# Performance work log

Measured on AMD Instinct MI355X. Metric: run time of the kernel, lower is better.

Reference implementation:

```python
import jax, jax.numpy as jnp
import numpy as np

HIDDEN = 2048
TOKENS = 16384


def setup_inputs() -> dict:
    key = jax.random.key(0)
    kx, kw, kb, kg, kbe = jax.random.split(key, 5)
    x = jax.random.normal(kx, (TOKENS, HIDDEN), dtype=jnp.float32)
    # LayerNorm affine params
    ln_gamma = jnp.ones((HIDDEN,), dtype=jnp.float32)
    ln_beta = jnp.zeros((HIDDEN,), dtype=jnp.float32)
    # Linear params (PyTorch default init scale ~ U(-1/sqrt(d), 1/sqrt(d)))
    bound = 1.0 / np.sqrt(HIDDEN)
    W = jax.random.uniform(kw, (HIDDEN, HIDDEN), minval=-bound, maxval=bound, dtype=jnp.float32)
    b = jax.random.uniform(kb, (HIDDEN,), minval=-bound, maxval=bound, dtype=jnp.float32)
    return {"x": x, "ln_gamma": ln_gamma, "ln_beta": ln_beta, "W": W, "b": b}


def reference(x, ln_gamma, ln_beta, W, b):
    eps = 1e-5
    mu = jnp.mean(x, axis=-1, keepdims=True)
    var = jnp.mean(jnp.square(x - mu), axis=-1, keepdims=True)
    xn = (x - mu) * jax.lax.rsqrt(var + eps) * ln_gamma + ln_beta
    # Linear: y = xn @ W^T + b (W stored as [out, in] like torch)
    y = jnp.einsum('td,od->to', xn, W) + b
    # torch F.gelu default = exact erf gelu
    return jax.nn.gelu(y, approximate=False)
```

## Files before the change

kernel.cpp:

```cpp
#include <hip/hip_runtime.h>
#include <math.h>

#define TOKENS 16384
#define HIDDEN 2048
#define BM 256
#define BN 256
#define BK 64
#define NT (HIDDEN / BK)

typedef __attribute__((ext_vector_type(4))) float f32x4;
typedef __attribute__((ext_vector_type(8))) short s16x8;

__device__ __forceinline__ unsigned short f2bf(float f) {
  unsigned int u = __float_as_uint(f);
  u += 0x7fffu + ((u >> 16) & 1u);
  return (unsigned short)(u >> 16);
}

__device__ __forceinline__ float fast_gelu(float y) {
  float t = y * fmaf(y * y, 0.044715f, 1.0f);
  float e = __builtin_amdgcn_exp2f(-2.3022082f * t);
  return y * __builtin_amdgcn_rcpf(1.0f + e);
}

__global__ __launch_bounds__(256) void wconv_kernel(const float* __restrict__ W,
                                                    unsigned short* __restrict__ Wb) {
  const int n4 = (HIDDEN * HIDDEN) / 4;
  for (int i = blockIdx.x * 256 + threadIdx.x; i < n4; i += gridDim.x * 256) {
    float4 v = *(const float4*)(W + (size_t)i * 4);
    ushort4 o;
    o.x = f2bf(v.x); o.y = f2bf(v.y); o.z = f2bf(v.z); o.w = f2bf(v.w);
    *(ushort4*)(Wb + (size_t)i * 4) = o;
  }
}

__global__ __launch_bounds__(256) void ln_kernel(const float* __restrict__ x,
                                                 const float* __restrict__ gamma,
                                                 const float* __restrict__ beta,
                                                 unsigned short* __restrict__ xn) {
  const int row = blockIdx.x;
  const int t = threadIdx.x;
  const int wave = t >> 6, lane = t & 63;
  const float* xr = x + (size_t)row * HIDDEN + t * 8;
  float4 v0 = *(const float4*)(xr);
  float4 v1 = *(const float4*)(xr + 4);
  float xv[8] = {v0.x, v0.y, v0.z, v0.w, v1.x, v1.y, v1.z, v1.w};

  float s = 0.f, ss = 0.f;
#pragma unroll
  for (int j = 0; j < 8; ++j) { s += xv[j]; ss = fmaf(xv[j], xv[j], ss); }

#pragma unroll
  for (int off = 32; off > 0; off >>= 1) {
    s += __shfl_xor(s, off, 64);
    ss += __shfl_xor(ss, off, 64);
  }
  __shared__ float rs[4], rss[4];
  if (lane == 0) { rs[wave] = s; rss[wave] = ss; }
  __syncthreads();
  s = rs[0] + rs[1] + rs[2] + rs[3];
  ss = rss[0] + rss[1] + rss[2] + rss[3];

  const float mean = s * (1.0f / HIDDEN);
  const float var = ss * (1.0f / HIDDEN) - mean * mean;
  const float rstd = rsqrtf(var + 1e-5f);

  float4 g0 = *(const float4*)(gamma + t * 8);
  float4 g1 = *(const float4*)(gamma + t * 8 + 4);
  float4 b0 = *(const float4*)(beta + t * 8);
  float4 b1 = *(const float4*)(beta + t * 8 + 4);
  float gv[8] = {g0.x, g0.y, g0.z, g0.w, g1.x, g1.y, g1.z, g1.w};
  float bv[8] = {b0.x, b0.y, b0.z, b0.w, b1.x, b1.y, b1.z, b1.w};

  union { unsigned short h[8]; uint4 q; } pk;
#pragma unroll
  for (int j = 0; j < 8; ++j)
    pk.h[j] = f2bf((xv[j] - mean) * rstd * gv[j] + bv[j]);
  *(uint4*)(xn + (size_t)row * HIDDEN + t * 8) = pk.q;
}


#define GLOAD(gp, lp) __builtin_amdgcn_global_load_lds( \
    (const __attribute__((address_space(1))) unsigned int*)(gp), \
    (__attribute__((address_space(3))) unsigned int*)(lp), 16, 0, 0)

__global__ __launch_bounds__(512, 1) void gemm_kernel(const unsigned short* __restrict__ A,
                                                      const unsigned short* __restrict__ B,
                                                      const float* __restrict__ bias,
                                                      float* __restrict__ out) {
  __shared__ __attribute__((aligned(16))) char lds[131072];

  const int tid = threadIdx.x;
  const int lane = tid & 63;
  const int wave = tid >> 6;
  const int fr = lane & 15, hi = lane >> 4;

  const int wg = blockIdx.x;
  const int swz = (wg & 7) * 64 + (wg >> 3);
  const int tm = swz >> 3, tn = swz & 7;
  const int row0 = tm * BM, col0 = tn * BN;

  const int wmi = wave >> 2;
  const int wni = wave & 3;
  const int hB = wni >> 1, gB = wni & 1;

  const int rho = tid >> 3, sig = tid & 7;
  const int colgrp = ((sig ^ (rho & 7)) << 3);
  const unsigned short* Ap = A + (size_t)(row0 + rho) * HIDDEN + colgrp;
  const unsigned short* Bp = B + (size_t)(col0 + ((rho >> 5) << 6) + (rho & 31)) * HIDDEN + colgrp;
  const int ldsWaveOff = wave << 10;

  const int s0 = ((hi ^ (fr & 7)) << 4);
  const int s1 = (((4 + hi) ^ (fr & 7)) << 4);
  const int aRowB = fr << 7;
  const int bRowB = (((gB << 5) + fr) << 7);

  auto stageA = [&](int tt, int bufd, int qm) {
    const int tc = tt < NT ? tt : NT - 1;
    const unsigned short* g = Ap + (size_t)(qm << 6) * HIDDEN + tc * BK;
    GLOAD(g, lds + ((((bufd << 2) | qm) << 13)) + ldsWaveOff);
    GLOAD(g + (size_t)128 * HIDDEN, lds + ((((bufd << 2) | 2 | qm) << 13)) + ldsWaveOff);
  };
  auto stageB = [&](int tt, int bufd, int qn) {
    const int tc = tt < NT ? tt : NT - 1;
    const unsigned short* g = Bp + (size_t)(qn << 5) * HIDDEN + tc * BK;
    GLOAD(g, lds + 65536 + ((((bufd << 2) | qn) << 13)) + ldsWaveOff);
    GLOAD(g + (size_t)128 * HIDDEN, lds + 65536 + ((((bufd << 2) | 2 | qn) << 13)) + ldsWaveOff);
  };

  f32x4 acc[2][4][4] = {};
  s16x8 a[4][2], b[2][2];

  stageA(0, 0, 0); stageB(0, 0, 1); stageA(0, 0, 1); stageB(0, 0, 0);
  stageA(1, 1, 0); stageB(1, 1, 1);
  asm volatile("s_waitcnt vmcnt(4)" ::: "memory");
  __builtin_amdgcn_s_barrier();

  for (int t = 0; t < NT; ++t) {
    const int buf = t & 1;
    const char* Abase = lds + (((buf << 2) | (wmi << 1)) << 13);
    const char* Bbase = lds + 65536 + (((buf << 2) | (hB << 1)) << 13);

#pragma unroll
    for (int mi = 0; mi < 4; ++mi) {
      a[mi][0] = *(const s16x8*)(Abase + mi * 2048 + aRowB + s0);
      a[mi][1] = *(const s16x8*)(Abase + mi * 2048 + aRowB + s1);
    }
#pragma unroll
    for (int nj = 0; nj < 2; ++nj) {
      b[nj][0] = *(const s16x8*)(Bbase + nj * 2048 + bRowB + s0);
      b[nj][1] = *(const s16x8*)(Bbase + nj * 2048 + bRowB + s1);
    }
    stageA(t + 1, buf ^ 1, 1);
    asm volatile("s_waitcnt lgkmcnt(8)" ::: "memory");
    __builtin_amdgcn_s_barrier();
    asm volatile("s_waitcnt lgkmcnt(0)" ::: "memory");
    __builtin_amdgcn_s_setprio(1);
#pragma unroll
    for (int mi = 0; mi < 4; ++mi)
#pragma unroll
      for (int nj = 0; nj < 2; ++nj)
#pragma unroll
        for (int kk = 0; kk < 2; ++kk)
          acc[0][mi][nj] = __builtin_amdgcn_mfma_f32_16x16x32_bf16(a[mi][kk], b[nj][kk], acc[0][mi][nj], 0, 0, 0);
    __builtin_amdgcn_s_setprio(0);
    __builtin_amdgcn_s_barrier();

#pragma unroll
    for (int nj = 0; nj < 2; ++nj) {
      b[nj][0] = *(const s16x8*)(Bbase + 8192 + nj * 2048 + bRowB + s0);
      b[nj][1] = *(const s16x8*)(Bbase + 8192 + nj * 2048 + bRowB + s1);
    }
    stageB(t + 1, buf ^ 1, 0);
    __builtin_amdgcn_s_barrier();
    asm volatile("s_waitcnt lgkmcnt(0)" ::: "memory");
    __builtin_amdgcn_s_setprio(1);
#pragma unroll
    for (int mi = 0; mi < 4; ++mi)
#pragma unroll
      for (int nj = 0; nj < 2; ++nj)
#pragma unroll
        for (int kk = 0; kk < 2; ++kk)
          acc[0][mi][2 + nj] = __builtin_amdgcn_mfma_f32_16x16x32_bf16(a[mi][kk], b[nj][kk], acc[0][mi][2 + nj], 0, 0, 0);
    __builtin_amdgcn_s_setprio(0);
    __builtin_amdgcn_s_barrier();

#pragma unroll
    for (int mi = 0; mi < 4; ++mi) {
      a[mi][0] = *(const s16x8*)(Abase + 8192 + mi * 2048 + aRowB + s0);
      a[mi][1] = *(const s16x8*)(Abase + 8192 + mi * 2048 + aRowB + s1);
    }
    stageA(t + 2, buf, 0);
    asm volatile("s_waitcnt lgkmcnt(4)" ::: "memory");
    __builtin_amdgcn_s_barrier();
    asm volatile("s_waitcnt lgkmcnt(0)" ::: "memory");
    __builtin_amdgcn_s_setprio(1);
#pragma unroll
    for (int mi = 0; mi < 4; ++mi)
#pragma unroll
      for (int nj = 0; nj < 2; ++nj)
#pragma unroll
        for (int kk = 0; kk < 2; ++kk)
          acc[1][mi][2 + nj] = __builtin_amdgcn_mfma_f32_16x16x32_bf16(a[mi][kk], b[nj][kk], acc[1][mi][2 + nj], 0, 0, 0);
    __builtin_amdgcn_s_setprio(0);
    __builtin_amdgcn_s_barrier();

#pragma unroll
    for (int nj = 0; nj < 2; ++nj) {
      b[nj][0] = *(const s16x8*)(Bbase + nj * 2048 + bRowB + s0);
      b[nj][1] = *(const s16x8*)(Bbase + nj * 2048 + bRowB + s1);
    }
    stageB(t + 2, buf, 1);
    asm volatile("s_waitcnt vmcnt(4)" ::: "memory");
    __builtin_amdgcn_s_barrier();
    asm volatile("s_waitcnt lgkmcnt(0)" ::: "memory");
    __builtin_amdgcn_s_setprio(1);
#pragma unroll
    for (int mi = 0; mi < 4; ++mi)
#pragma unroll
      for (int nj = 0; nj < 2; ++nj)
#pragma unroll
        for (int kk = 0; kk < 2; ++kk)
          acc[1][mi][nj] = __builtin_amdgcn_mfma_f32_16x16x32_bf16(a[mi][kk], b[nj][kk], acc[1][mi][nj], 0, 0, 0);
    __builtin_amdgcn_s_setprio(0);
    __builtin_amdgcn_s_barrier();
  }

  asm volatile("s_waitcnt vmcnt(0)" ::: "memory");

  float bcol[4];
#pragma unroll
  for (int ni = 0; ni < 4; ++ni)
    bcol[ni] = bias[col0 + (wni << 6) + ni * 16 + fr];

#pragma unroll
  for (int qm = 0; qm < 2; ++qm)
#pragma unroll
    for (int mi = 0; mi < 4; ++mi)
#pragma unroll
      for (int ni = 0; ni < 4; ++ni) {
        const int c = col0 + (wni << 6) + ni * 16 + fr;
#pragma unroll
        for (int j = 0; j < 4; ++j) {
          const int r = row0 + wmi * 128 + qm * 64 + mi * 16 + hi * 4 + j;
          float y = acc[qm][mi][ni][j] + bcol[ni];
          out[(size_t)r * HIDDEN + c] = fast_gelu(y);
        }
      }
}

extern "C" void kernel_launch(void* const* d_in, const int* in_sizes, int n_in,
                              void* d_out, int out_size, void* d_ws, size_t ws_size,
                              hipStream_t stream) {
  const float* x     = (const float*)d_in[0];
  const float* gamma = (const float*)d_in[1];
  const float* beta  = (const float*)d_in[2];
  const float* W     = (const float*)d_in[3];
  const float* bias  = (const float*)d_in[4];
  float* out = (float*)d_out;

  unsigned short* xn = (unsigned short*)d_ws;
  unsigned short* wb = (unsigned short*)((char*)d_ws + (size_t)TOKENS * HIDDEN * 2);

  hipLaunchKernelGGL(wconv_kernel, dim3(1024), dim3(256), 0, stream, W, wb);
  hipLaunchKernelGGL(ln_kernel, dim3(TOKENS), dim3(256), 0, stream, x, gamma, beta, xn);
  hipLaunchKernelGGL(gemm_kernel, dim3((TOKENS / BM) * (HIDDEN / BN)), dim3(512), 0, stream,
                     xn, wb, bias, out);
}
```

Measured before the change: 176.2 us.

## Make GEMM workgroups process two row tiles sequentially with continuous pipeline

The GEMM grid is halved so each workgroup computes two output tiles, 8192 rows apart, sharing the same column block. The K-loop runs over both tiles back to back, keeping the LDS prefetch pipeline going across the boundary, and the first tile's epilogue is flushed mid-loop. This targets the tail effect of 512 single-wave workgroups on 256 CUs (exactly two waves) and the per-tile pipeline warmup. The cost is that the first tile's epilogue stores now stall the pipeline mid-loop, and the swizzle mapping changes.

```diff
diff --git a/kernel.cpp b/kernel.cpp
--- a/kernel.cpp
+++ b/kernel.cpp
@@ -7,6 +7,8 @@
 #define BN 256
 #define BK 64
 #define NT (HIDDEN / BK)
+#define NVT (2 * NT)
+#define PASS_ROWS (32 * BM)
 
 typedef __attribute__((ext_vector_type(4))) float f32x4;
 typedef __attribute__((ext_vector_type(8))) short s16x8;
@@ -96,7 +98,7 @@
   const int fr = lane & 15, hi = lane >> 4;
 
   const int wg = blockIdx.x;
-  const int swz = (wg & 7) * 64 + (wg >> 3);
+  const int swz = (wg & 7) * 32 + (wg >> 3);
   const int tm = swz >> 3, tn = swz & 7;
   const int row0 = tm * BM, col0 = tn * BN;
 
@@ -115,28 +117,50 @@
   const int aRowB = fr << 7;
   const int bRowB = (((gB << 5) + fr) << 7);
 
-  auto stageA = [&](int tt, int bufd, int qm) {
-    const int tc = tt < NT ? tt : NT - 1;
-    const unsigned short* g = Ap + (size_t)(qm << 6) * HIDDEN + tc * BK;
+  auto stageA = [&](int vt, int bufd, int qm) {
+    const int vc = vt < NVT ? vt : NVT - 1;
+    const unsigned short* g = Ap + (size_t)(vc >> 5) * ((size_t)PASS_ROWS * HIDDEN)
+                                 + (size_t)(qm << 6) * HIDDEN + (vc & 31) * BK;
     GLOAD(g, lds + ((((bufd << 2) | qm) << 13)) + ldsWaveOff);
     GLOAD(g + (size_t)128 * HIDDEN, lds + ((((bufd << 2) | 2 | qm) << 13)) + ldsWaveOff);
   };
-  auto stageB = [&](int tt, int bufd, int qn) {
-    const int tc = tt < NT ? tt : NT - 1;
-    const unsigned short* g = Bp + (size_t)(qn << 5) * HIDDEN + tc * BK;
+  auto stageB = [&](int vt, int bufd, int qn) {
+    const int vc = vt < NVT ? vt : NVT - 1;
+    const unsigned short* g = Bp + (size_t)(qn << 5) * HIDDEN + (vc & 31) * BK;
     GLOAD(g, lds + 65536 + ((((bufd << 2) | qn) << 13)) + ldsWaveOff);
     GLOAD(g + (size_t)128 * HIDDEN, lds + 65536 + ((((bufd << 2) | 2 | qn) << 13)) + ldsWaveOff);
   };
 
   f32x4 acc[2][4][4] = {};
   s16x8 a[4][2], b[2][2];
+
+  auto flush = [&](int pass) {
+    float bcol[4];
+#pragma unroll
+    for (int ni = 0; ni < 4; ++ni)
+      bcol[ni] = bias[col0 + (wni << 6) + ni * 16 + fr];
+#pragma unroll
+    for (int qm = 0; qm < 2; ++qm)
+#pragma unroll
+      for (int mi = 0; mi < 4; ++mi)
+#pragma unroll
+        for (int ni = 0; ni < 4; ++ni) {
+          const int c = col0 + (wni << 6) + ni * 16 + fr;
+#pragma unroll
+          for (int j = 0; j < 4; ++j) {
+            const int r = row0 + pass * PASS_ROWS + wmi * 128 + qm * 64 + mi * 16 + hi * 4 + j;
+            float y = acc[qm][mi][ni][j] + bcol[ni];
+            out[(size_t)r * HIDDEN + c] = fast_gelu(y);
+          }
+        }
+  };
 
   stageA(0, 0, 0); stageB(0, 0, 1); stageA(0, 0, 1); stageB(0, 0, 0);
   stageA(1, 1, 0); stageB(1, 1, 1);
   asm volatile("s_waitcnt vmcnt(4)" ::: "memory");
   __builtin_amdgcn_s_barrier();
 
-  for (int t = 0; t < NT; ++t) {
+  for (int t = 0; t < NVT; ++t) {
     const int buf = t & 1;
     const char* Abase = lds + (((buf << 2) | (wmi << 1)) << 13);
     const char* Bbase = lds + 65536 + (((buf << 2) | (hB << 1)) << 13);
@@ -224,29 +248,21 @@
           acc[1][mi][nj] = __builtin_amdgcn_mfma_f32_16x16x32_bf16(a[mi][kk], b[nj][kk], acc[1][mi][nj], 0, 0, 0);
     __builtin_amdgcn_s_setprio(0);
     __builtin_amdgcn_s_barrier();
+
+    if (t == NT - 1) {
+      flush(0);
+#pragma unroll
+      for (int qm = 0; qm < 2; ++qm)
+#pragma unroll
+        for (int mi = 0; mi < 4; ++mi)
+#pragma unroll
+          for (int ni = 0; ni < 4; ++ni)
+            acc[qm][mi][ni] = (f32x4){0.f, 0.f, 0.f, 0.f};
+    }
   }
 
   asm volatile("s_waitcnt vmcnt(0)" ::: "memory");
-
-  float bcol[4];
-#pragma unroll
-  for (int ni = 0; ni < 4; ++ni)
-    bcol[ni] = bias[col0 + (wni << 6) + ni * 16 + fr];
-
-#pragma unroll
-  for (int qm = 0; qm < 2; ++qm)
-#pragma unroll
-    for (int mi = 0; mi < 4; ++mi)
-#pragma unroll
-      for (int ni = 0; ni < 4; ++ni) {
-        const int c = col0 + (wni << 6) + ni * 16 + fr;
-#pragma unroll
-        for (int j = 0; j < 4; ++j) {
-          const int r = row0 + wmi * 128 + qm * 64 + mi * 16 + hi * 4 + j;
-          float y = acc[qm][mi][ni][j] + bcol[ni];
-          out[(size_t)r * HIDDEN + c] = fast_gelu(y);
-        }
-      }
+  flush(1);
 }
 
 extern "C" void kernel_launch(void* const* d_in, const int* in_sizes, int n_in,
@@ -264,6 +280,6 @@
 
   hipLaunchKernelGGL(wconv_kernel, dim3(1024), dim3(256), 0, stream, W, wb);
   hipLaunchKernelGGL(ln_kernel, dim3(TOKENS), dim3(256), 0, stream, x, gamma, beta, xn);
-  hipLaunchKernelGGL(gemm_kernel, dim3((TOKENS / BM) * (HIDDEN / BN)), dim3(512), 0, stream,
+  hipLaunchKernelGGL(gemm_kernel, dim3((TOKENS / BM / 2) * (HIDDEN / BN)), dim3(512), 0, stream,
                      xn, wb, bias, out);
 }
```

New measurement: 201.5 us. 1.14x slower.

## Hold full B fragment in registers and merge four MFMA phases into two

Applied to the files above, without the earlier changes.

Each wave now loads all four B sub-tiles into registers at the start of the iteration and reuses them for both A halves. This cuts the per-iteration loop from four LDS-load/barrier/MFMA phases to two, and loads B from LDS once instead of twice. Global staging is reordered to match: both B halves are issued before A, with adjusted vmcnt waits. The cost is more vector registers for the B fragments and larger MFMA bursts with fewer interleaving points for overlapping loads, which could lower occupancy or expose latency.

```diff
diff --git a/kernel.cpp b/kernel.cpp
--- a/kernel.cpp
+++ b/kernel.cpp
@@ -129,11 +129,11 @@
   };
 
   f32x4 acc[2][4][4] = {};
-  s16x8 a[4][2], b[2][2];
-
-  stageA(0, 0, 0); stageB(0, 0, 1); stageA(0, 0, 1); stageB(0, 0, 0);
-  stageA(1, 1, 0); stageB(1, 1, 1);
-  asm volatile("s_waitcnt vmcnt(4)" ::: "memory");
+  s16x8 a[4][2], b[4][2];
+
+  stageB(0, 0, 0); stageB(0, 0, 1); stageA(0, 0, 0); stageA(0, 0, 1);
+  stageB(1, 1, 0); stageB(1, 1, 1); stageA(1, 1, 0);
+  asm volatile("s_waitcnt vmcnt(6)" ::: "memory");
   __builtin_amdgcn_s_barrier();
 
   for (int t = 0; t < NT; ++t) {
@@ -147,9 +147,10 @@
       a[mi][1] = *(const s16x8*)(Abase + mi * 2048 + aRowB + s1);
     }
 #pragma unroll
-    for (int nj = 0; nj < 2; ++nj) {
-      b[nj][0] = *(const s16x8*)(Bbase + nj * 2048 + bRowB + s0);
-      b[nj][1] = *(const s16x8*)(Bbase + nj * 2048 + bRowB + s1);
+    for (int nj = 0; nj < 4; ++nj) {
+      const char* bq = Bbase + (nj >> 1) * 8192 + (nj & 1) * 2048 + bRowB;
+      b[nj][0] = *(const s16x8*)(bq + s0);
+      b[nj][1] = *(const s16x8*)(bq + s1);
     }
     stageA(t + 1, buf ^ 1, 1);
     asm volatile("s_waitcnt lgkmcnt(8)" ::: "memory");
@@ -159,29 +160,10 @@
 #pragma unroll
     for (int mi = 0; mi < 4; ++mi)
 #pragma unroll
-      for (int nj = 0; nj < 2; ++nj)
+      for (int nj = 0; nj < 4; ++nj)
 #pragma unroll
         for (int kk = 0; kk < 2; ++kk)
           acc[0][mi][nj] = __builtin_amdgcn_mfma_f32_16x16x32_bf16(a[mi][kk], b[nj][kk], acc[0][mi][nj], 0, 0, 0);
-    __builtin_amdgcn_s_setprio(0);
-    __builtin_amdgcn_s_barrier();
-
-#pragma unroll
-    for (int nj = 0; nj < 2; ++nj) {
-      b[nj][0] = *(const s16x8*)(Bbase + 8192 + nj * 2048 + bRowB + s0);
-      b[nj][1] = *(const s16x8*)(Bbase + 8192 + nj * 2048 + bRowB + s1);
-    }
-    stageB(t + 1, buf ^ 1, 0);
-    __builtin_amdgcn_s_barrier();
-    asm volatile("s_waitcnt lgkmcnt(0)" ::: "memory");
-    __builtin_amdgcn_s_setprio(1);
-#pragma unroll
-    for (int mi = 0; mi < 4; ++mi)
-#pragma unroll
-      for (int nj = 0; nj < 2; ++nj)
-#pragma unroll
-        for (int kk = 0; kk < 2; ++kk)
-          acc[0][mi][2 + nj] = __builtin_amdgcn_mfma_f32_16x16x32_bf16(a[mi][kk], b[nj][kk], acc[0][mi][2 + nj], 0, 0, 0);
     __builtin_amdgcn_s_setprio(0);
     __builtin_amdgcn_s_barrier();
 
@@ -190,35 +172,17 @@
       a[mi][0] = *(const s16x8*)(Abase + 8192 + mi * 2048 + aRowB + s0);
       a[mi][1] = *(const s16x8*)(Abase + 8192 + mi * 2048 + aRowB + s1);
     }
+    stageB(t + 2, buf, 0);
+    stageB(t + 2, buf, 1);
     stageA(t + 2, buf, 0);
-    asm volatile("s_waitcnt lgkmcnt(4)" ::: "memory");
+    asm volatile("s_waitcnt vmcnt(6) lgkmcnt(4)" ::: "memory");
     __builtin_amdgcn_s_barrier();
     asm volatile("s_waitcnt lgkmcnt(0)" ::: "memory");
     __builtin_amdgcn_s_setprio(1);
 #pragma unroll
     for (int mi = 0; mi < 4; ++mi)
 #pragma unroll
-      for (int nj = 0; nj < 2; ++nj)
-#pragma unroll
-        for (int kk = 0; kk < 2; ++kk)
-          acc[1][mi][2 + nj] = __builtin_amdgcn_mfma_f32_16x16x32_bf16(a[mi][kk], b[nj][kk], acc[1][mi][2 + nj], 0, 0, 0);
-    __builtin_amdgcn_s_setprio(0);
-    __builtin_amdgcn_s_barrier();
-
-#pragma unroll
-    for (int nj = 0; nj < 2; ++nj) {
-      b[nj][0] = *(const s16x8*)(Bbase + nj * 2048 + bRowB + s0);
-      b[nj][1] = *(const s16x8*)(Bbase + nj * 2048 + bRowB + s1);
-    }
-    stageB(t + 2, buf, 1);
-    asm volatile("s_waitcnt vmcnt(4)" ::: "memory");
-    __builtin_amdgcn_s_barrier();
-    asm volatile("s_waitcnt lgkmcnt(0)" ::: "memory");
-    __builtin_amdgcn_s_setprio(1);
-#pragma unroll
-    for (int mi = 0; mi < 4; ++mi)
-#pragma unroll
-      for (int nj = 0; nj < 2; ++nj)
+      for (int nj = 0; nj < 4; ++nj)
 #pragma unroll
         for (int kk = 0; kk < 2; ++kk)
           acc[1][mi][nj] = __builtin_amdgcn_mfma_f32_16x16x32_bf16(a[mi][kk], b[nj][kk], acc[1][mi][nj], 0, 0, 0);
```

Measured after the change: 180.4 us. 2.3% more time.

## Switch GEMM inner loop to 32x32x16 bf16 MFMA tiles

Applied to the files above, without the earlier changes.

Replaces the 16x16x32 MFMA fragments with 32x32x16 MFMA instructions, restructuring the LDS fragment loads (four k-slices per operand), the accumulator layout and the epilogue row/column mapping to match. Larger MFMA tiles mean fewer LDS reads per flop and fewer instructions. It also removes the XCD-aware workgroup swizzle and uses a plain row-major tile order, which may change L2 locality across chiplets.

```diff
diff --git a/kernel.cpp b/kernel.cpp
--- a/kernel.cpp
+++ b/kernel.cpp
@@ -9,6 +9,7 @@
 #define NT (HIDDEN / BK)
 
 typedef __attribute__((ext_vector_type(4))) float f32x4;
+typedef __attribute__((ext_vector_type(16))) float f32x16;
 typedef __attribute__((ext_vector_type(8))) short s16x8;
 
 __device__ __forceinline__ unsigned short f2bf(float f) {
@@ -93,11 +94,10 @@
   const int tid = threadIdx.x;
   const int lane = tid & 63;
   const int wave = tid >> 6;
-  const int fr = lane & 15, hi = lane >> 4;
+  const int l31 = lane & 31, hi32 = lane >> 5;
 
   const int wg = blockIdx.x;
-  const int swz = (wg & 7) * 64 + (wg >> 3);
-  const int tm = swz >> 3, tn = swz & 7;
+  const int tm = wg >> 3, tn = wg & 7;
   const int row0 = tm * BM, col0 = tn * BN;
 
   const int wmi = wave >> 2;
@@ -110,10 +110,13 @@
   const unsigned short* Bp = B + (size_t)(col0 + ((rho >> 5) << 6) + (rho & 31)) * HIDDEN + colgrp;
   const int ldsWaveOff = wave << 10;
 
-  const int s0 = ((hi ^ (fr & 7)) << 4);
-  const int s1 = (((4 + hi) ^ (fr & 7)) << 4);
-  const int aRowB = fr << 7;
-  const int bRowB = (((gB << 5) + fr) << 7);
+  int aoff[4], boff[4];
+#pragma unroll
+  for (int ks = 0; ks < 4; ++ks) {
+    const int sb = (((2 * ks + hi32) ^ (lane & 7)) << 4);
+    aoff[ks] = (l31 << 7) + sb;
+    boff[ks] = (((gB << 5) + l31) << 7) + sb;
+  }
 
   auto stageA = [&](int tt, int bufd, int qm) {
     const int tc = tt < NT ? tt : NT - 1;
@@ -128,8 +131,8 @@
     GLOAD(g + (size_t)128 * HIDDEN, lds + 65536 + ((((bufd << 2) | 2 | qn) << 13)) + ldsWaveOff);
   };
 
-  f32x4 acc[2][4][4] = {};
-  s16x8 a[4][2], b[2][2];
+  f32x16 acc[4][2] = {};
+  s16x8 a[2][4], b[4];
 
   stageA(0, 0, 0); stageB(0, 0, 1); stageA(0, 0, 1); stageB(0, 0, 0);
   stageA(1, 1, 0); stageB(1, 1, 1);
@@ -142,111 +145,95 @@
     const char* Bbase = lds + 65536 + (((buf << 2) | (hB << 1)) << 13);
 
 #pragma unroll
-    for (int mi = 0; mi < 4; ++mi) {
-      a[mi][0] = *(const s16x8*)(Abase + mi * 2048 + aRowB + s0);
-      a[mi][1] = *(const s16x8*)(Abase + mi * 2048 + aRowB + s1);
-    }
-#pragma unroll
-    for (int nj = 0; nj < 2; ++nj) {
-      b[nj][0] = *(const s16x8*)(Bbase + nj * 2048 + bRowB + s0);
-      b[nj][1] = *(const s16x8*)(Bbase + nj * 2048 + bRowB + s1);
-    }
+    for (int mi = 0; mi < 2; ++mi)
+#pragma unroll
+      for (int ks = 0; ks < 4; ++ks)
+        a[mi][ks] = *(const s16x8*)(Abase + mi * 4096 + aoff[ks]);
+#pragma unroll
+    for (int ks = 0; ks < 4; ++ks)
+      b[ks] = *(const s16x8*)(Bbase + boff[ks]);
     stageA(t + 1, buf ^ 1, 1);
     asm volatile("s_waitcnt lgkmcnt(8)" ::: "memory");
     __builtin_amdgcn_s_barrier();
     asm volatile("s_waitcnt lgkmcnt(0)" ::: "memory");
     __builtin_amdgcn_s_setprio(1);
 #pragma unroll
-    for (int mi = 0; mi < 4; ++mi)
-#pragma unroll
-      for (int nj = 0; nj < 2; ++nj)
-#pragma unroll
-        for (int kk = 0; kk < 2; ++kk)
-          acc[0][mi][nj] = __builtin_amdgcn_mfma_f32_16x16x32_bf16(a[mi][kk], b[nj][kk], acc[0][mi][nj], 0, 0, 0);
-    __builtin_amdgcn_s_setprio(0);
-    __builtin_amdgcn_s_barrier();
-
-#pragma unroll
-    for (int nj = 0; nj < 2; ++nj) {
-      b[nj][0] = *(const s16x8*)(Bbase + 8192 + nj * 2048 + bRowB + s0);
-      b[nj][1] = *(const s16x8*)(Bbase + 8192 + nj * 2048 + bRowB + s1);
-    }
+    for (int mi = 0; mi < 2; ++mi)
+#pragma unroll
+      for (int ks = 0; ks < 4; ++ks)
+        acc[mi][0] = __builtin_amdgcn_mfma_f32_32x32x16_bf16(a[mi][ks], b[ks], acc[mi][0], 0, 0, 0);
+    __builtin_amdgcn_s_setprio(0);
+    __builtin_amdgcn_s_barrier();
+
+#pragma unroll
+    for (int ks = 0; ks < 4; ++ks)
+      b[ks] = *(const s16x8*)(Bbase + 8192 + boff[ks]);
     stageB(t + 1, buf ^ 1, 0);
     __builtin_amdgcn_s_barrier();
     asm volatile("s_waitcnt lgkmcnt(0)" ::: "memory");
     __builtin_amdgcn_s_setprio(1);
 #pragma unroll
-    for (int mi = 0; mi < 4; ++mi)
-#pragma unroll
-      for (int nj = 0; nj < 2; ++nj)
-#pragma unroll
-        for (int kk = 0; kk < 2; ++kk)
-          acc[0][mi][2 + nj] = __builtin_amdgcn_mfma_f32_16x16x32_bf16(a[mi][kk], b[nj][kk], acc[0][mi][2 + nj], 0, 0, 0);
-    __builtin_amdgcn_s_setprio(0);
-    __builtin_amdgcn_s_barrier();
-
-#pragma unroll
-    for (int mi = 0; mi < 4; ++mi) {
-      a[mi][0] = *(const s16x8*)(Abase + 8192 + mi * 2048 + aRowB + s0);
-      a[mi][1] = *(const s16x8*)(Abase + 8192 + mi * 2048 + aRowB + s1);
-    }
+    for (int mi = 0; mi < 2; ++mi)
+#pragma unroll
+      for (int ks = 0; ks < 4; ++ks)
+        acc[mi][1] = __builtin_amdgcn_mfma_f32_32x32x16_bf16(a[mi][ks], b[ks], acc[mi][1], 0, 0, 0);
+    __builtin_amdgcn_s_setprio(0);
+    __builtin_amdgcn_s_barrier();
+
+#pragma unroll
+    for (int mi = 0; mi < 2; ++mi)
+#pragma unroll
+      for (int ks = 0; ks < 4; ++ks)
+        a[mi][ks] = *(const s16x8*)(Abase + 8192 + mi * 4096 + aoff[ks]);
     stageA(t + 2, buf, 0);
     asm volatile("s_waitcnt lgkmcnt(4)" ::: "memory");
     __builtin_amdgcn_s_barrier();
     asm volatile("s_waitcnt lgkmcnt(0)" ::: "memory");
     __builtin_amdgcn_s_setprio(1);
 #pragma unroll
-    for (int mi = 0; mi < 4; ++mi)
-#pragma unroll
-      for (int nj = 0; nj < 2; ++nj)
-#pragma unroll
-        for (int kk = 0; kk < 2; ++kk)
-          acc[1][mi][2 + nj] = __builtin_amdgcn_mfma_f32_16x16x32_bf16(a[mi][kk], b[nj][kk], acc[1][mi][2 + nj], 0, 0, 0);
-    __builtin_amdgcn_s_setprio(0);
-    __builtin_amdgcn_s_barrier();
-
-#pragma unroll
-    for (int nj = 0; nj < 2; ++nj) {
-      b[nj][0] = *(const s16x8*)(Bbase + nj * 2048 + bRowB + s0);
-      b[nj][1] = *(const s16x8*)(Bbase + nj * 2048 + bRowB + s1);
-    }
+    for (int mi = 0; mi < 2; ++mi)
+#pragma unroll
+      for (int ks = 0; ks < 4; ++ks)
+        acc[2 + mi][1] = __builtin_amdgcn_mfma_f32_32x32x16_bf16(a[mi][ks], b[ks], acc[2 + mi][1], 0, 0, 0);
+    __builtin_amdgcn_s_setprio(0);
+    __builtin_amdgcn_s_barrier();
+
+#pragma unroll
+    for (int ks = 0; ks < 4; ++ks)
+      b[ks] = *(const s16x8*)(Bbase + boff[ks]);
     stageB(t + 2, buf, 1);
     asm volatile("s_waitcnt vmcnt(4)" ::: "memory");
     __builtin_amdgcn_s_barrier();
     asm volatile("s_waitcnt lgkmcnt(0)" ::: "memory");
     __builtin_amdgcn_s_setprio(1);
 #pragma unroll
-    for (int mi = 0; mi < 4; ++mi)
-#pragma unroll
-      for (int nj = 0; nj < 2; ++nj)
-#pragma unroll
-        for (int kk = 0; kk < 2; ++kk)
-          acc[1][mi][nj] = __builtin_amdgcn_mfma_f32_16x16x32_bf16(a[mi][kk], b[nj][kk], acc[1][mi][nj], 0, 0, 0);
+    for (int mi = 0; mi < 2; ++mi)
+#pragma unroll
+      for (int ks = 0; ks < 4; ++ks)
+        acc[2 + mi][0] = __builtin_amdgcn_mfma_f32_32x32x16_bf16(a[mi][ks], b[ks], acc[2 + mi][0], 0, 0, 0);
     __builtin_amdgcn_s_setprio(0);
     __builtin_amdgcn_s_barrier();
   }
 
   asm volatile("s_waitcnt vmcnt(0)" ::: "memory");
 
-  float bcol[4];
-#pragma unroll
-  for (int ni = 0; ni < 4; ++ni)
-    bcol[ni] = bias[col0 + (wni << 6) + ni * 16 + fr];
-
-#pragma unroll
-  for (int qm = 0; qm < 2; ++qm)
-#pragma unroll
-    for (int mi = 0; mi < 4; ++mi)
-#pragma unroll
-      for (int ni = 0; ni < 4; ++ni) {
-        const int c = col0 + (wni << 6) + ni * 16 + fr;
-#pragma unroll
-        for (int j = 0; j < 4; ++j) {
-          const int r = row0 + wmi * 128 + qm * 64 + mi * 16 + hi * 4 + j;
-          float y = acc[qm][mi][ni][j] + bcol[ni];
-          out[(size_t)r * HIDDEN + c] = fast_gelu(y);
-        }
+  float bcol[2];
+#pragma unroll
+  for (int qn = 0; qn < 2; ++qn)
+    bcol[qn] = bias[col0 + (wni << 6) + qn * 32 + l31];
+
+#pragma unroll
+  for (int mi = 0; mi < 4; ++mi)
+#pragma unroll
+    for (int qn = 0; qn < 2; ++qn) {
+      const int c = col0 + (wni << 6) + qn * 32 + l31;
+#pragma unroll
+      for (int reg = 0; reg < 16; ++reg) {
+        const int r = row0 + wmi * 128 + mi * 32 + (reg & 3) + 8 * (reg >> 2) + 4 * hi32;
+        float y = acc[mi][qn][reg] + bcol[qn];
+        out[(size_t)r * HIDDEN + c] = fast_gelu(y);
       }
+    }
 }
 
 extern "C" void kernel_launch(void* const* d_in, const int* in_sizes, int n_in,
```

Result: slower. 200.5 us (+13.8%).
